# Performance work log

Measured on AMD Instinct MI355X. Metric: run time of the kernel, lower is better.

The kernel has to match this reference:

```python
import jax, jax.numpy as jnp
import numpy as np

NUM_CLASSES = 81
NEG_RATIO = 3
POS_FRAC = 0.03  # realistic fraction of positive (matched) anchors


def setup_inputs() -> dict:
    key = jax.random.key(0)
    k1, k2, k3, k4, k5 = jax.random.split(key, 5)
    B, A, C = 64, 8732, NUM_CLASSES
    pred_loc = jax.random.normal(k1, (B, A, 4), dtype=jnp.float32)
    pred_conf = jax.random.normal(k2, (B, A, C), dtype=jnp.float32)
    gt_loc = jax.random.normal(k3, (B, A, 4), dtype=jnp.float32)
    raw_cls = jax.random.randint(k4, (B, A), 1, C)
    is_pos = jax.random.uniform(k5, (B, A)) < POS_FRAC
    gt_label = jnp.where(is_pos, raw_cls, 0).astype(jnp.int32)
    return {"pred_loc": pred_loc, "pred_conf": pred_conf, "gt_loc": gt_loc, "gt_label": gt_label}


def reference(pred_loc, pred_conf, gt_loc, gt_label):
    # pred_loc/gt_loc: [B, A, 4]; pred_conf: [B, A, C]; gt_label: [B, A] int
    pos = gt_label > 0  # [B, A]

    # Smooth L1 (beta=1), summed over positive anchors only (mask instead of boolean gather)
    d = jnp.abs(pred_loc - gt_loc)
    sl1 = jnp.where(d < 1.0, 0.5 * d * d, d - 0.5)
    loc_loss = jnp.sum(sl1 * pos[..., None].astype(sl1.dtype))

    # Per-anchor cross-entropy
    logp = jax.nn.log_softmax(pred_conf, axis=-1)  # [B, A, C]
    ce = -jnp.take_along_axis(logp, gt_label[..., None].astype(jnp.int32), axis=-1)[..., 0]  # [B, A]

    cef = ce.reshape(-1)
    posf = pos.reshape(-1)
    num_pos = jnp.sum(posf)
    num_neg = jnp.minimum(NEG_RATIO * num_pos, posf.size - num_pos)

    # Hard-negative mining: rank negatives by CE descending; select top num_neg.
    neg_vals = jnp.where(posf, -jnp.inf, cef)
    order = jnp.argsort(-neg_vals)  # indices sorted by descending negative loss
    rank = jnp.zeros_like(order).at[order].set(jnp.arange(order.size))
    neg_sel = (rank < num_neg) & (~posf)

    pos_conf_loss = jnp.sum(jnp.where(posf, cef, 0.0))
    neg_conf_loss = jnp.sum(jnp.where(neg_sel, cef, 0.0))

    total = (loc_loss + pos_conf_loss + neg_conf_loss) / num_pos.astype(cef.dtype)
    return total
```

## Files before the change

kernel.cpp:

```cpp
#include <hip/hip_runtime.h>
#include <hip/hip_bf16.h>
#include <math.h>

#define NB   64
#define NA   8732
#define NCLS 81
#define NTOT (NB * NA)
#define NTILE (NTOT / 16)
#define NBIN  2048
#define CSCALE 64.0f
#define NSLICE 16
#define K1BLK  4096
#define SUMBLK 256

#define OFF_KEYS   0
#define OFF_HISTA  (NTOT * 4)
#define OFF_SCAL   (OFF_HISTA + NSLICE * NBIN * 4)
#define OFF_PBNP   (OFF_SCAL + 64)
#define OFF_PBPC   (OFF_PBNP + K1BLK * 4)
#define OFF_PBNEG  (OFF_PBPC + K1BLK * 4)
#define OFF_PBLOC  (OFF_PBNEG + SUMBLK * 4)
#define OFF_PBBIN  (OFF_PBLOC + SUMBLK * 4)
#define ZERO_BYTES (NSLICE * NBIN * 4 + 64)

#define DPPF(v, ctrl) \
  __int_as_float(__builtin_amdgcn_update_dpp(0, __float_as_int(v), ctrl, 0xF, 0xF, true))

__global__ __launch_bounds__(256, 5) void mbl_k1(
    const float* __restrict__ pred_conf, const int* __restrict__ gt_label,
    float* __restrict__ keys, unsigned* __restrict__ hista,
    unsigned* __restrict__ pb_np, float* __restrict__ pb_pc) {
  __shared__ float srow[4][1312];
  __shared__ unsigned lhist[NBIN];
  __shared__ float s_pc[4];
  __shared__ unsigned s_np[4];
  for (int i = threadIdx.x; i < NBIN; i += 256) lhist[i] = 0u;
  __syncthreads();

  const int lane = threadIdx.x & 63;
  const int wid  = threadIdx.x >> 6;
  const int gw   = (blockIdx.x << 2) + wid;
  const int l    = lane & 3;
  const int q    = lane >> 2;
  float* slice = srow[wid];
  float4* s4 = (float4*)slice;

  float posconf = 0.f;
  unsigned npos = 0u;

  for (int tile = gw; tile < NTILE; tile += K1BLK * 4) {
    const float4* src = (const float4*)pred_conf + (unsigned)tile * 324u;
    const float4 r0 = src[lane];
    const float4 r1 = src[lane + 64];
    const float4 r2 = src[lane + 128];
    const float4 r3 = src[lane + 192];
    const float4 r4 = src[lane + 256];
    float4 r5;
    if (lane < 4) r5 = src[lane + 320];
    const int lab = gt_label[(tile << 4) + q];

    s4[lane]       = r0;
    s4[lane + 64]  = r1;
    s4[lane + 128] = r2;
    s4[lane + 192] = r3;
    s4[lane + 256] = r4;
    if (lane < 4) s4[lane + 320] = r5;

    const int rb = q * 81;
    float e = 0.f;
#pragma unroll
    for (int j = 0; j < 20; ++j) e += __expf(slice[rb + l + 4 * j]);
    if (l == 0) e += __expf(slice[rb + 80]);
    e += DPPF(e, 0xB1);
    e += DPPF(e, 0x4E);
    const float pick = slice[rb + lab];

    if (l == 0) {
      const float ce = __logf(e) - pick;
      const int a = (tile << 4) + q;
      if (lab > 0) {
        npos += 1u; posconf += ce; keys[a] = -1.f;
      } else {
        keys[a] = ce;
        int bin = (int)(ce * CSCALE);
        bin = min(bin, NBIN - 1);
        atomicAdd(&lhist[bin], 1u);
      }
    }
  }

#pragma unroll
  for (int s = 1; s < 64; s <<= 1) {
    posconf += __shfl_xor(posconf, s);
    npos    += (unsigned)__shfl_xor((int)npos, s);
  }
  if ((threadIdx.x & 63) == 0) { s_pc[wid] = posconf; s_np[wid] = npos; }
  __syncthreads();
  if (threadIdx.x == 0) {
    pb_pc[blockIdx.x] = s_pc[0] + s_pc[1] + s_pc[2] + s_pc[3];
    pb_np[blockIdx.x] = s_np[0] + s_np[1] + s_np[2] + s_np[3];
  }
  const unsigned slice_off = (blockIdx.x & (NSLICE - 1)) * NBIN;
  for (int i = threadIdx.x; i < NBIN; i += 256) {
    const unsigned v = lhist[i];
    if (v) atomicAdd(&hista[slice_off + i], v);
  }
}

__global__ __launch_bounds__(256) void mbl_sel(const unsigned* __restrict__ hista,
                                               const unsigned* __restrict__ pb_np,
                                               const float* __restrict__ pb_pc,
                                               unsigned* __restrict__ scal_u,
                                               float* __restrict__ scal_f) {
  __shared__ unsigned hbin[NBIN];
  __shared__ unsigned partial[256];
  __shared__ float q_pc[4];
  __shared__ unsigned q_np[4];
  __shared__ unsigned s_k;
  const int t = threadIdx.x;

  unsigned np = 0u; float pc = 0.f;
  for (int i = t; i < K1BLK; i += 256) { np += pb_np[i]; pc += pb_pc[i]; }
#pragma unroll
  for (int s = 1; s < 64; s <<= 1) {
    np += (unsigned)__shfl_xor((int)np, s);
    pc += __shfl_xor(pc, s);
  }
  if ((t & 63) == 0) { q_np[t >> 6] = np; q_pc[t >> 6] = pc; }
  __syncthreads();
  if (t == 0) {
    const unsigned tot = q_np[0] + q_np[1] + q_np[2] + q_np[3];
    scal_u[0] = tot;
    scal_f[2] = q_pc[0] + q_pc[1] + q_pc[2] + q_pc[3];
    const unsigned k = min(3u * tot, (unsigned)NTOT - tot);
    s_k = k; scal_u[4] = k;
    if (k == 0u) { scal_u[5] = NBIN; scal_u[6] = 0u; scal_u[7] = 1u; }
  }
  __syncthreads();
  const unsigned k = s_k;
  if (k == 0u) return;

  unsigned s = 0u;
#pragma unroll
  for (int j = 0; j < 8; ++j) {
    unsigned v = 0u;
#pragma unroll
    for (int sl = 0; sl < NSLICE; ++sl) v += hista[sl * NBIN + t * 8 + j];
    hbin[t * 8 + j] = v;
    s += v;
  }
  unsigned val = s;
  partial[t] = val;
  __syncthreads();
  for (int off = 1; off < 256; off <<= 1) {
    const unsigned add = (t + off < 256) ? partial[t + off] : 0u;
    __syncthreads();
    val += add;
    partial[t] = val;
    __syncthreads();
  }
  const unsigned suf = val - s;
  if (suf < k && k <= suf + s) {
    unsigned c = suf;
    for (int b = 7; b >= 0; --b) {
      const unsigned hb = hbin[t * 8 + b];
      if (c + hb >= k) {
        scal_u[5] = (unsigned)(t * 8 + b);
        scal_u[6] = k - c;
        scal_u[7] = hb;
        break;
      }
      c += hb;
    }
  }
}

__global__ __launch_bounds__(256) void mbl_sum(
    const float* __restrict__ keys, const int* __restrict__ gt_label,
    const float* __restrict__ pred_loc, const float* __restrict__ gt_loc,
    const unsigned* __restrict__ scal_u,
    float* __restrict__ pb_neg, float* __restrict__ pb_loc,
    float* __restrict__ pb_bin) {
  __shared__ float q_n[4], q_l[4], q_b[4];
  const int bstar = (int)scal_u[5];
  float acc = 0.f, lacc = 0.f, bacc = 0.f;
  const int stride = gridDim.x * 256;
  for (int i = blockIdx.x * 256 + threadIdx.x; i < NTOT; i += stride) {
    const float kf = keys[i];
    if (kf >= 0.f) {
      int b = (int)(kf * CSCALE);
      b = min(b, NBIN - 1);
      if (b > bstar) acc += kf;
      else if (b == bstar) bacc += kf;
    }
    const int lb = gt_label[i];
    if (lb > 0) {
      const float4 pl = ((const float4*)pred_loc)[i];
      const float4 gl = ((const float4*)gt_loc)[i];
      float d;
      d = fabsf(pl.x - gl.x); lacc += (d < 1.f) ? 0.5f * d * d : d - 0.5f;
      d = fabsf(pl.y - gl.y); lacc += (d < 1.f) ? 0.5f * d * d : d - 0.5f;
      d = fabsf(pl.z - gl.z); lacc += (d < 1.f) ? 0.5f * d * d : d - 0.5f;
      d = fabsf(pl.w - gl.w); lacc += (d < 1.f) ? 0.5f * d * d : d - 0.5f;
    }
  }
#pragma unroll
  for (int s = 1; s < 64; s <<= 1) {
    acc  += __shfl_xor(acc, s);
    lacc += __shfl_xor(lacc, s);
    bacc += __shfl_xor(bacc, s);
  }
  const int wv = threadIdx.x >> 6;
  if ((threadIdx.x & 63) == 0) { q_n[wv] = acc; q_l[wv] = lacc; q_b[wv] = bacc; }
  __syncthreads();
  if (threadIdx.x == 0) {
    pb_neg[blockIdx.x] = q_n[0] + q_n[1] + q_n[2] + q_n[3];
    pb_loc[blockIdx.x] = q_l[0] + q_l[1] + q_l[2] + q_l[3];
    pb_bin[blockIdx.x] = q_b[0] + q_b[1] + q_b[2] + q_b[3];
  }
}

__global__ __launch_bounds__(256) void mbl_fin(const unsigned* __restrict__ scal_u,
                                               const float* __restrict__ scal_f,
                                               const float* __restrict__ pb_neg,
                                               const float* __restrict__ pb_loc,
                                               const float* __restrict__ pb_bin,
                                               float* __restrict__ out) {
  __shared__ float q_n[4], q_l[4], q_b[4];
  const int t = threadIdx.x;
  float n = pb_neg[t], l = pb_loc[t], b = pb_bin[t];
#pragma unroll
  for (int s = 1; s < 64; s <<= 1) {
    n += __shfl_xor(n, s);
    l += __shfl_xor(l, s);
    b += __shfl_xor(b, s);
  }
  const int wv = t >> 6;
  if ((t & 63) == 0) { q_n[wv] = n; q_l[wv] = l; q_b[wv] = b; }
  __syncthreads();
  if (t == 0) {
    float negsum = q_n[0] + q_n[1] + q_n[2] + q_n[3];
    const float locsum = q_l[0] + q_l[1] + q_l[2] + q_l[3];
    const float binsum = q_b[0] + q_b[1] + q_b[2] + q_b[3];
    const unsigned r = scal_u[6];
    if (r > 0u) negsum += (float)r * (binsum / (float)scal_u[7]);
    out[0] = (locsum + scal_f[2] + negsum) / (float)scal_u[0];
  }
}

extern "C" void kernel_launch(void* const* d_in, const int* in_sizes, int n_in,
                              void* d_out, int out_size, void* d_ws, size_t ws_size,
                              hipStream_t stream) {
  const float* pred_loc  = (const float*)d_in[0];
  const float* pred_conf = (const float*)d_in[1];
  const float* gt_loc    = (const float*)d_in[2];
  const int*   gt_label  = (const int*)d_in[3];
  float* out = (float*)d_out;

  char* ws = (char*)d_ws;
  float*    keys   = (float*)(ws + OFF_KEYS);
  unsigned* hista  = (unsigned*)(ws + OFF_HISTA);
  unsigned* scal_u = (unsigned*)(ws + OFF_SCAL);
  float*    scal_f = (float*)(ws + OFF_SCAL);
  unsigned* pb_np  = (unsigned*)(ws + OFF_PBNP);
  float*    pb_pc  = (float*)(ws + OFF_PBPC);
  float*    pb_neg = (float*)(ws + OFF_PBNEG);
  float*    pb_loc = (float*)(ws + OFF_PBLOC);
  float*    pb_bin = (float*)(ws + OFF_PBBIN);

  hipMemsetAsync(ws + OFF_HISTA, 0, ZERO_BYTES, stream);

  mbl_k1<<<K1BLK, 256, 0, stream>>>(pred_conf, gt_label, keys, hista, pb_np, pb_pc);
  mbl_sel<<<1, 256, 0, stream>>>(hista, pb_np, pb_pc, scal_u, scal_f);
  mbl_sum<<<SUMBLK, 256, 0, stream>>>(keys, gt_label, pred_loc, gt_loc, scal_u,
                                      pb_neg, pb_loc, pb_bin);
  mbl_fin<<<1, 256, 0, stream>>>(scal_u, scal_f, pb_neg, pb_loc, pb_bin, out);
}
```

Measured before the change: 70.48 us.

## Load logits directly to registers with double-buffered prefetch, drop LDS staging

Each lane now reads its 20 logits of a row straight from global memory with unaligned float4 loads instead of staging the tile through shared memory. The label pick is done with register compares and a DPP reduction. Two register sets alternate so the next tile's loads are issued before the current tile is computed, and occupancy is raised from 5 to 6 blocks per SM. This removes the LDS round trip and hides memory latency, at the cost of more registers, uncoalesced 4-byte-aligned accesses and extra compare instructions.

```diff
diff --git a/kernel.cpp b/kernel.cpp
--- a/kernel.cpp
+++ b/kernel.cpp
@@ -26,11 +26,13 @@
 #define DPPF(v, ctrl) \
   __int_as_float(__builtin_amdgcn_update_dpp(0, __float_as_int(v), ctrl, 0xF, 0xF, true))
 
-__global__ __launch_bounds__(256, 5) void mbl_k1(
+typedef float f4 __attribute__((ext_vector_type(4)));
+typedef f4 __attribute__((aligned(4))) f4u;
+
+__global__ __launch_bounds__(256, 6) void mbl_k1(
     const float* __restrict__ pred_conf, const int* __restrict__ gt_label,
     float* __restrict__ keys, unsigned* __restrict__ hista,
     unsigned* __restrict__ pb_np, float* __restrict__ pb_pc) {
-  __shared__ float srow[4][1312];
   __shared__ unsigned lhist[NBIN];
   __shared__ float s_pc[4];
   __shared__ unsigned s_np[4];
@@ -42,52 +44,75 @@
   const int gw   = (blockIdx.x << 2) + wid;
   const int l    = lane & 3;
   const int q    = lane >> 2;
-  float* slice = srow[wid];
-  float4* s4 = (float4*)slice;
+  const char* cbase = (const char*)pred_conf;
 
   float posconf = 0.f;
   unsigned npos = 0u;
 
-  for (int tile = gw; tile < NTILE; tile += K1BLK * 4) {
-    const float4* src = (const float4*)pred_conf + (unsigned)tile * 324u;
-    const float4 r0 = src[lane];
-    const float4 r1 = src[lane + 64];
-    const float4 r2 = src[lane + 128];
-    const float4 r3 = src[lane + 192];
-    const float4 r4 = src[lane + 256];
-    float4 r5;
-    if (lane < 4) r5 = src[lane + 320];
-    const int lab = gt_label[(tile << 4) + q];
-
-    s4[lane]       = r0;
-    s4[lane + 64]  = r1;
-    s4[lane + 128] = r2;
-    s4[lane + 192] = r3;
-    s4[lane + 256] = r4;
-    if (lane < 4) s4[lane + 320] = r5;
-
-    const int rb = q * 81;
-    float e = 0.f;
-#pragma unroll
-    for (int j = 0; j < 20; ++j) e += __expf(slice[rb + l + 4 * j]);
-    if (l == 0) e += __expf(slice[rb + 80]);
-    e += DPPF(e, 0xB1);
-    e += DPPF(e, 0x4E);
-    const float pick = slice[rb + lab];
-
-    if (l == 0) {
-      const float ce = __logf(e) - pick;
-      const int a = (tile << 4) + q;
-      if (lab > 0) {
-        npos += 1u; posconf += ce; keys[a] = -1.f;
-      } else {
-        keys[a] = ce;
-        int bin = (int)(ce * CSCALE);
-        bin = min(bin, NBIN - 1);
-        atomicAdd(&lhist[bin], 1u);
-      }
-    }
-  }
+  f4 A0, A1, A2, A3, A4; float Ax; int Alab;
+  f4 B0, B1, B2, B3, B4; float Bx; int Blab;
+
+#define LOADS(r0, r1, r2, r3, r4, rx, rlab, tt) do {                           \
+    const int _a = ((tt) << 4) + q;                                            \
+    const char* _p = cbase + (unsigned)_a * 324u + (l << 4);                   \
+    r0 = *(const f4u*)(_p);                                                    \
+    r1 = *(const f4u*)(_p + 64);                                               \
+    r2 = *(const f4u*)(_p + 128);                                              \
+    r3 = *(const f4u*)(_p + 192);                                              \
+    r4 = *(const f4u*)(_p + 256);                                              \
+    rx = (l == 0) ? *(const float*)(cbase + (unsigned)_a * 324u + 320u) : 0.f; \
+    rlab = gt_label[_a];                                                       \
+  } while (0)
+
+#define COMPUTE(r0, r1, r2, r3, r4, rx, rlab, tt) do {                         \
+    float e = 0.f, pk = 0.f;                                                   \
+    const int _b = (l << 2);     \
+    _Pragma("unroll")                                                          \
+    for (int _m = 0; _m < 4; ++_m) {                                           \
+      e += __expf(r0[_m]) + __expf(r1[_m]) + __expf(r2[_m])                    \
+         + __expf(r3[_m]) + __expf(r4[_m]);                                    \
+      if (rlab == _b + _m)      pk = r0[_m];                                   \
+      if (rlab == _b + 16 + _m) pk = r1[_m];                                   \
+      if (rlab == _b + 32 + _m) pk = r2[_m];                                   \
+      if (rlab == _b + 48 + _m) pk = r3[_m];                                   \
+      if (rlab == _b + 64 + _m) pk = r4[_m];                                   \
+    }                                                                          \
+    if (l == 0) {                                                              \
+      e += __expf(rx);                                                         \
+      if (rlab == 80) pk = rx;                                                 \
+    }                                                                          \
+    e += DPPF(e, 0xB1);  pk += DPPF(pk, 0xB1);                                 \
+    e += DPPF(e, 0x4E);  pk += DPPF(pk, 0x4E);                                 \
+    if (l == 0) {                                                              \
+      const float ce = __logf(e) - pk;                               \
+      const int _a = ((tt) << 4) + q;                                          \
+      if (rlab > 0) {                                                          \
+        npos += 1u; posconf += ce; keys[_a] = -1.f;                            \
+      } else {                                                                 \
+        keys[_a] = ce;                                                         \
+        int _bin = (int)(ce * CSCALE);                                         \
+        _bin = min(_bin, NBIN - 1);                                            \
+        atomicAdd(&lhist[_bin], 1u);                                           \
+      }                                                                        \
+    }                                                                          \
+  } while (0)
+
+  int i0 = gw;
+  const int G = K1BLK * 4;
+  bool v0 = i0 < NTILE;
+  if (v0) LOADS(A0, A1, A2, A3, A4, Ax, Alab, i0);
+  while (v0) {
+    const int i1 = i0 + G; const bool v1 = i1 < NTILE;
+    if (v1) LOADS(B0, B1, B2, B3, B4, Bx, Blab, i1);
+    COMPUTE(A0, A1, A2, A3, A4, Ax, Alab, i0);
+    if (!v1) break;
+    const int i2 = i1 + G; const bool v2 = i2 < NTILE;
+    if (v2) LOADS(A0, A1, A2, A3, A4, Ax, Alab, i2);
+    COMPUTE(B0, B1, B2, B3, B4, Bx, Blab, i1);
+    i0 = i2; v0 = v2;
+  }
+#undef LOADS
+#undef COMPUTE
 
 #pragma unroll
   for (int s = 1; s < 64; s <<= 1) {
```

After: 67.43 us. -4.3%, faster.
